# Kernel tuning notes

Measured on AMD Instinct MI355X. Metric: run time of the kernel, lower is better.

## Reference

```python
import jax, jax.numpy as jnp
import numpy as np

B = 32768
D_MODEL = 1024
N_TIERS = 3
TOP_K = 2
GATE_INIT_STD = 0.02


def setup_inputs() -> dict:
    key = jax.random.key(0)
    k1, k2, k3 = jax.random.split(key, 3)
    tier_outputs = jax.random.normal(k1, (B, N_TIERS, D_MODEL), dtype=jnp.float32)
    query = jax.random.normal(k2, (B, D_MODEL), dtype=jnp.float32)
    W = jax.random.normal(k3, (N_TIERS, D_MODEL), dtype=jnp.float32) * GATE_INIT_STD
    return {"tier_outputs": tier_outputs, "query": query, "W": W}


def reference(tier_outputs, query, W):
    # query is detached in the torch module before the gate projection
    q = jax.lax.stop_gradient(query)
    router_logits = jnp.einsum("bd,td->bt", q, W)           # (B, n_tiers)
    topk_vals, topk_idx = jax.lax.top_k(router_logits, TOP_K)  # (B, top_k)
    topk_weights = jax.nn.softmax(topk_vals, axis=-1)          # (B, top_k)
    # scatter soft weights back into dense (B, n_tiers); inactive tiers stay 0
    rows = jnp.arange(router_logits.shape[0])[:, None]
    gate_weights = jnp.zeros_like(router_logits).at[rows, topk_idx].set(topk_weights)
    # masked weighted sum over tiers (inactive tiers have weight 0)
    merged = jnp.einsum("btd,bt->bd", tier_outputs, gate_weights)  # (B, d_model)
    return merged, gate_weights, router_logits
```

## Files before the change

kernel.cpp:

```cpp
#include <hip/hip_runtime.h>
#include <math.h>

#define BATCH   32768
#define DMODEL  1024
#define NTIERS  3

__global__ __launch_bounds__(256) void sparse_router_kernel(
    const float* __restrict__ tier_outputs,
    const float* __restrict__ query,
    const float* __restrict__ W,
    float* __restrict__ merged,
    float* __restrict__ gate,
    float* __restrict__ logits_out)
{
    const int b   = blockIdx.x;
    const int tid = threadIdx.x;

    const float4* q4 = reinterpret_cast<const float4*>(query + (size_t)b * DMODEL);
    const float4  q  = q4[tid];

    const float4* w4 = reinterpret_cast<const float4*>(W);
    const float4  w0 = w4[tid];
    const float4  w1 = w4[tid + DMODEL / 4];
    const float4  w2 = w4[tid + 2 * DMODEL / 4];

    float p0 = q.x * w0.x + q.y * w0.y + q.z * w0.z + q.w * w0.w;
    float p1 = q.x * w1.x + q.y * w1.y + q.z * w1.z + q.w * w1.w;
    float p2 = q.x * w2.x + q.y * w2.y + q.z * w2.z + q.w * w2.w;

    #pragma unroll
    for (int off = 32; off >= 1; off >>= 1) {
        p0 += __shfl_down(p0, off);
        p1 += __shfl_down(p1, off);
        p2 += __shfl_down(p2, off);
    }

    __shared__ float red0[4], red1[4], red2[4];
    __shared__ float s_w[2];
    __shared__ int   s_i[2];

    const int wave = tid >> 6;
    const int lane = tid & 63;
    if (lane == 0) { red0[wave] = p0; red1[wave] = p1; red2[wave] = p2; }
    __syncthreads();

    if (tid == 0) {
        float l[NTIERS];
        l[0] = red0[0] + red0[1] + red0[2] + red0[3];
        l[1] = red1[0] + red1[1] + red1[2] + red1[3];
        l[2] = red2[0] + red2[1] + red2[2] + red2[3];

        int i0 = 0;
        if (l[1] > l[i0]) i0 = 1;
        if (l[2] > l[i0]) i0 = 2;
        int i1 = -1;
        #pragma unroll
        for (int t = 0; t < NTIERS; ++t) {
            if (t == i0) continue;
            if (i1 < 0 || l[t] > l[i1]) i1 = t;
        }

        const float v0 = l[i0];
        const float v1 = l[i1];
        const float e1 = expf(v1 - v0);
        const float inv = 1.0f / (1.0f + e1);
        const float g0 = inv;
        const float g1 = e1 * inv;

        float gd[NTIERS] = {0.0f, 0.0f, 0.0f};
        gd[i0] = g0;
        gd[i1] = g1;

        const size_t o3 = (size_t)b * NTIERS;
        logits_out[o3 + 0] = l[0];
        logits_out[o3 + 1] = l[1];
        logits_out[o3 + 2] = l[2];
        gate[o3 + 0] = gd[0];
        gate[o3 + 1] = gd[1];
        gate[o3 + 2] = gd[2];

        s_w[0] = g0; s_w[1] = g1;
        s_i[0] = i0; s_i[1] = i1;
    }
    __syncthreads();

    const float gA = s_w[0];
    const float gB = s_w[1];
    const size_t baseA = ((size_t)b * NTIERS + s_i[0]) * DMODEL;
    const size_t baseB = ((size_t)b * NTIERS + s_i[1]) * DMODEL;

    const float4 a = reinterpret_cast<const float4*>(tier_outputs + baseA)[tid];
    const float4 c = reinterpret_cast<const float4*>(tier_outputs + baseB)[tid];

    float4 m;
    m.x = gA * a.x + gB * c.x;
    m.y = gA * a.y + gB * c.y;
    m.z = gA * a.z + gB * c.z;
    m.w = gA * a.w + gB * c.w;

    reinterpret_cast<float4*>(merged + (size_t)b * DMODEL)[tid] = m;
}

extern "C" void kernel_launch(void* const* d_in, const int* in_sizes, int n_in,
                              void* d_out, int out_size, void* d_ws, size_t ws_size,
                              hipStream_t stream) {
    const float* tier_outputs = (const float*)d_in[0];
    const float* query        = (const float*)d_in[1];
    const float* W            = (const float*)d_in[2];

    float* out = (float*)d_out;
    float* merged     = out;
    float* gate       = out + (size_t)BATCH * DMODEL;
    float* logits_out = gate + (size_t)BATCH * NTIERS;

    sparse_router_kernel<<<BATCH, 256, 0, stream>>>(
        tier_outputs, query, W, merged, gate, logits_out);
}
```

Baseline: 99.71 us.

## Map one wavefront per row and drop block-level reductions and barriers

Each 64-lane wavefront now handles a whole batch row, so a block of 256 threads covers four rows. The logit dot products are reduced with xor shuffles inside the wave, and every lane gets the top-2 softmax weights directly. This removes the shared-memory reduction, the two __syncthreads barriers and the single-thread serial section. It also adds nontemporal loads and stores for the streamed query, tier and merged data, and raises per-lane register use with four float4 loads per stream.

```diff
diff --git a/kernel.cpp b/kernel.cpp
--- a/kernel.cpp
+++ b/kernel.cpp
@@ -4,6 +4,10 @@
 #define BATCH   32768
 #define DMODEL  1024
 #define NTIERS  3
+#define F4_PER_ROW (DMODEL / 4)
+#define F4_PER_LANE 4
+
+typedef float f32x4 __attribute__((ext_vector_type(4)));
 
 __global__ __launch_bounds__(256) void sparse_router_kernel(
     const float* __restrict__ tier_outputs,
@@ -13,92 +17,78 @@
     float* __restrict__ gate,
     float* __restrict__ logits_out)
 {
-    const int b   = blockIdx.x;
-    const int tid = threadIdx.x;
+    const int wave = threadIdx.x >> 6;
+    const int lane = threadIdx.x & 63;
+    const int b    = blockIdx.x * 4 + wave;
 
-    const float4* q4 = reinterpret_cast<const float4*>(query + (size_t)b * DMODEL);
-    const float4  q  = q4[tid];
+    const f32x4* q4 = reinterpret_cast<const f32x4*>(query + (size_t)b * DMODEL);
+    f32x4 q[F4_PER_LANE];
+    #pragma unroll
+    for (int j = 0; j < F4_PER_LANE; ++j)
+        q[j] = __builtin_nontemporal_load(&q4[j * 64 + lane]);
 
-    const float4* w4 = reinterpret_cast<const float4*>(W);
-    const float4  w0 = w4[tid];
-    const float4  w1 = w4[tid + DMODEL / 4];
-    const float4  w2 = w4[tid + 2 * DMODEL / 4];
-
-    float p0 = q.x * w0.x + q.y * w0.y + q.z * w0.z + q.w * w0.w;
-    float p1 = q.x * w1.x + q.y * w1.y + q.z * w1.z + q.w * w1.w;
-    float p2 = q.x * w2.x + q.y * w2.y + q.z * w2.z + q.w * w2.w;
+    const f32x4* w4 = reinterpret_cast<const f32x4*>(W);
+    float p0 = 0.f, p1 = 0.f, p2 = 0.f;
+    #pragma unroll
+    for (int j = 0; j < F4_PER_LANE; ++j) {
+        const f32x4 w0 = w4[0 * F4_PER_ROW + j * 64 + lane];
+        const f32x4 w1 = w4[1 * F4_PER_ROW + j * 64 + lane];
+        const f32x4 w2 = w4[2 * F4_PER_ROW + j * 64 + lane];
+        p0 += q[j].x * w0.x + q[j].y * w0.y + q[j].z * w0.z + q[j].w * w0.w;
+        p1 += q[j].x * w1.x + q[j].y * w1.y + q[j].z * w1.z + q[j].w * w1.w;
+        p2 += q[j].x * w2.x + q[j].y * w2.y + q[j].z * w2.z + q[j].w * w2.w;
+    }
 
     #pragma unroll
-    for (int off = 32; off >= 1; off >>= 1) {
-        p0 += __shfl_down(p0, off);
-        p1 += __shfl_down(p1, off);
-        p2 += __shfl_down(p2, off);
+    for (int off = 1; off <= 32; off <<= 1) {
+        p0 += __shfl_xor(p0, off);
+        p1 += __shfl_xor(p1, off);
+        p2 += __shfl_xor(p2, off);
     }
 
-    __shared__ float red0[4], red1[4], red2[4];
-    __shared__ float s_w[2];
-    __shared__ int   s_i[2];
+    float l[NTIERS] = {p0, p1, p2};
+    int i0 = 0;
+    if (l[1] > l[i0]) i0 = 1;
+    if (l[2] > l[i0]) i0 = 2;
+    int i1 = -1;
+    #pragma unroll
+    for (int t = 0; t < NTIERS; ++t) {
+        if (t == i0) continue;
+        if (i1 < 0 || l[t] > l[i1]) i1 = t;
+    }
 
-    const int wave = tid >> 6;
-    const int lane = tid & 63;
-    if (lane == 0) { red0[wave] = p0; red1[wave] = p1; red2[wave] = p2; }
-    __syncthreads();
+    const float e1  = expf(l[i1] - l[i0]);
+    const float inv = 1.0f / (1.0f + e1);
+    const float g0  = inv;
+    const float g1  = e1 * inv;
 
-    if (tid == 0) {
-        float l[NTIERS];
-        l[0] = red0[0] + red0[1] + red0[2] + red0[3];
-        l[1] = red1[0] + red1[1] + red1[2] + red1[3];
-        l[2] = red2[0] + red2[1] + red2[2] + red2[3];
+    if (lane < NTIERS) {
+        const size_t o3 = (size_t)b * NTIERS + lane;
+        logits_out[o3] = l[lane];
+        gate[o3]       = (lane == i0) ? g0 : (lane == i1) ? g1 : 0.0f;
+    }
 
-        int i0 = 0;
-        if (l[1] > l[i0]) i0 = 1;
-        if (l[2] > l[i0]) i0 = 2;
-        int i1 = -1;
-        #pragma unroll
-        for (int t = 0; t < NTIERS; ++t) {
-            if (t == i0) continue;
-            if (i1 < 0 || l[t] > l[i1]) i1 = t;
-        }
+    const f32x4* tA = reinterpret_cast<const f32x4*>(
+        tier_outputs + ((size_t)b * NTIERS + i0) * DMODEL);
+    const f32x4* tB = reinterpret_cast<const f32x4*>(
+        tier_outputs + ((size_t)b * NTIERS + i1) * DMODEL);
+    f32x4* mo = reinterpret_cast<f32x4*>(merged + (size_t)b * DMODEL);
 
-        const float v0 = l[i0];
-        const float v1 = l[i1];
-        const float e1 = expf(v1 - v0);
-        const float inv = 1.0f / (1.0f + e1);
-        const float g0 = inv;
-        const float g1 = e1 * inv;
-
-        float gd[NTIERS] = {0.0f, 0.0f, 0.0f};
-        gd[i0] = g0;
-        gd[i1] = g1;
-
-        const size_t o3 = (size_t)b * NTIERS;
-        logits_out[o3 + 0] = l[0];
-        logits_out[o3 + 1] = l[1];
-        logits_out[o3 + 2] = l[2];
-        gate[o3 + 0] = gd[0];
-        gate[o3 + 1] = gd[1];
-        gate[o3 + 2] = gd[2];
-
-        s_w[0] = g0; s_w[1] = g1;
-        s_i[0] = i0; s_i[1] = i1;
+    f32x4 a[F4_PER_LANE], c[F4_PER_LANE];
+    #pragma unroll
+    for (int j = 0; j < F4_PER_LANE; ++j) {
+        a[j] = __builtin_nontemporal_load(&tA[j * 64 + lane]);
+        c[j] = __builtin_nontemporal_load(&tB[j * 64 + lane]);
     }
-    __syncthreads();
-
-    const float gA = s_w[0];
-    const float gB = s_w[1];
-    const size_t baseA = ((size_t)b * NTIERS + s_i[0]) * DMODEL;
-    const size_t baseB = ((size_t)b * NTIERS + s_i[1]) * DMODEL;
-
-    const float4 a = reinterpret_cast<const float4*>(tier_outputs + baseA)[tid];
-    const float4 c = reinterpret_cast<const float4*>(tier_outputs + baseB)[tid];
-
-    float4 m;
-    m.x = gA * a.x + gB * c.x;
-    m.y = gA * a.y + gB * c.y;
-    m.z = gA * a.z + gB * c.z;
-    m.w = gA * a.w + gB * c.w;
-
-    reinterpret_cast<float4*>(merged + (size_t)b * DMODEL)[tid] = m;
+    #pragma unroll
+    for (int j = 0; j < F4_PER_LANE; ++j) {
+        f32x4 m;
+        m.x = g0 * a[j].x + g1 * c[j].x;
+        m.y = g0 * a[j].y + g1 * c[j].y;
+        m.z = g0 * a[j].z + g1 * c[j].z;
+        m.w = g0 * a[j].w + g1 * c[j].w;
+        __builtin_nontemporal_store(m, &mo[j * 64 + lane]);
+    }
 }
 
 extern "C" void kernel_launch(void* const* d_in, const int* in_sizes, int n_in,
@@ -113,6 +103,6 @@
     float* gate       = out + (size_t)BATCH * DMODEL;
     float* logits_out = gate + (size_t)BATCH * NTIERS;
 
-    sparse_router_kernel<<<BATCH, 256, 0, stream>>>(
+    sparse_router_kernel<<<BATCH / 4, 256, 0, stream>>>(
         tier_outputs, query, W, merged, gate, logits_out);
 }
```

Result: faster. 88.31 us (-11.4%).
